# Performance work log

Hardware: AMD Instinct MI355X
Metric: run time of the kernel (lower is better)

Reference implementation:

```python
import jax, jax.numpy as jnp
import numpy as np

B, L, F, H, K = 2048, 256, 64, 32, 2  # batch, seq len, features, g_hidden, LocalHilDim

def _dense_init(key, fan_in, fan_out):
    return (jax.random.normal(key, (fan_in, fan_out), jnp.float32) / np.sqrt(fan_in).astype(np.float32))

def setup_inputs() -> dict:
    key = jax.random.key(0)
    ks = jax.random.split(key, 12)
    s = jax.random.randint(ks[0], (B, L), 0, K)
    g = jax.random.normal(ks[1], (B,), jnp.float32)
    return dict(
        s=s, g=g,
        W_emb=_dense_init(ks[2], K, F), b_emb=jnp.zeros((F,), jnp.float32),
        W_g1=_dense_init(ks[3], 1, H), b_g1=jnp.zeros((H,), jnp.float32),
        W_g2=_dense_init(ks[4], H, F), b_g2=jnp.zeros((F,), jnp.float32),
        W_gh=_dense_init(ks[5], 1, F), b_gh=jnp.zeros((F,), jnp.float32),
        W_gc=_dense_init(ks[6], 1, F), b_gc=jnp.zeros((F,), jnp.float32),
        Wi=_dense_init(ks[7], F, 4 * F),  # fused input->gates (flax LSTMCell ii/if/ig/io, no bias)
        Wh=_dense_init(ks[8], F, 4 * F),  # fused hidden->gates (hi/hf/hg/ho)
        b_lstm=jnp.zeros((4 * F,), jnp.float32),  # fused gate biases
        W_amp=_dense_init(ks[9], F, K), b_amp=jnp.zeros((K,), jnp.float32),
    )

def reference(s, g, W_emb, b_emb, W_g1, b_g1, W_g2, b_g2, W_gh, b_gh, W_gc, b_gc, Wi, Wh, b_lstm, W_amp, b_amp):
    logProbFactor = 1.0
    g_in = g[:, None]                                            # [B,1]
    g_vec = jnp.tanh(g_in @ W_g1 + b_g1) @ W_g2 + b_g2          # g_mlp -> [B,F]
    h0 = g_in @ W_gh + b_gh                                      # init_carry h [B,F]
    c0 = g_in @ W_gc + b_gc                                      # init_carry c [B,F]
    s_pad = jnp.pad(s, ((0, 0), (1, 0)))                         # [B,L+1], leading 0 token
    seqy = jax.nn.one_hot(s_pad, K, dtype=jnp.float32)           # [B,L+1,K]
    emb = seqy @ W_emb + b_emb + g_vec[:, None, :]               # [B,L+1,F]
    # precompute input-side gate projections once: [B,L+1,4F]
    x_proj = emb @ Wi + b_lstm

    def step(carry, xt):                                         # xt: [B,4F]
        h, c = carry
        z = xt + h @ Wh
        zi, zf, zg, zo = jnp.split(z, 4, axis=-1)
        c = jax.nn.sigmoid(zf) * c + jax.nn.sigmoid(zi) * jnp.tanh(zg)
        h = jax.nn.sigmoid(zo) * jnp.tanh(c)
        return (h, c), h

    _, ys = jax.lax.scan(step, (h0, c0), jnp.swapaxes(x_proj, 0, 1))  # ys: [L+1,B,F]
    y = jnp.swapaxes(ys, 0, 1)                                   # [B,L+1,F]
    logits = y[:, :-1, :] @ W_amp + b_amp                        # [B,L,K]
    logp = jax.nn.log_softmax(logits) * logProbFactor
    token_logp = jnp.take_along_axis(logp, s[..., None], axis=-1)[..., 0]  # [B,L]
    return token_logp.sum(axis=-1)                               # [B]
```

## Files before the change

kernel.cpp:

```cpp
#include <hip/hip_runtime.h>


typedef __attribute__((ext_vector_type(8))) short bf16x8;
typedef __attribute__((ext_vector_type(4))) float f32x4;

#define L2E 1.44269504088896340736f
#define LN2 0.69314718055994530942f

__device__ __forceinline__ short f2bf(float x) {
    unsigned u = __builtin_bit_cast(unsigned, x);
    unsigned r = (u + 0x7FFFu + ((u >> 16) & 1u)) >> 16;
    return (short)r;
}

__global__ __launch_bounds__(256) void lstm_kernel(
    const int* __restrict__ s, const float* __restrict__ g,
    const float* __restrict__ W_emb, const float* __restrict__ b_emb,
    const float* __restrict__ W_g1, const float* __restrict__ b_g1,
    const float* __restrict__ W_g2, const float* __restrict__ b_g2,
    const float* __restrict__ W_gh, const float* __restrict__ b_gh,
    const float* __restrict__ W_gc, const float* __restrict__ b_gc,
    const float* __restrict__ Wi, const float* __restrict__ Wh,
    const float* __restrict__ b_lstm, const float* __restrict__ W_amp,
    const float* __restrict__ b_amp, float* __restrict__ out)
{
    __shared__ float Bx[35 * 256];
    __shared__ unsigned char sp_l[260];
    __shared__ __align__(16) short Hb[2][320];
    __shared__ float red[4][4];

    const int tid = threadIdx.x;
    const int w   = tid >> 6;
    const int l   = tid & 63;
    const int n2  = l & 15;
    const int q   = l >> 4;
    const int wgb = blockIdx.x * 4;

    {
        const int n = tid;
        const float sc = (n >= 128 && n < 192) ? (-2.0f * L2E) : (-L2E);
        float acc[35];
        #pragma unroll
        for (int i = 0; i < 35; ++i) acc[i] = 0.f;
        for (int f = 0; f < 64; ++f) {
            float wi = Wi[f * 256 + n] * sc;
            #pragma unroll
            for (int k = 0; k < 32; ++k) acc[k] += W_g2[k * 64 + f] * wi;
            acc[32] += W_emb[f] * wi;
            acc[33] += W_emb[64 + f] * wi;
            acc[34] += (b_emb[f] + b_g2[f]) * wi;
        }
        acc[34] += b_lstm[n] * sc;
        #pragma unroll
        for (int i = 0; i < 35; ++i) Bx[i * 256 + n] = acc[i];
    }
    {
        unsigned v = 0;
        #pragma unroll
        for (int b = 0; b < 4; ++b)
            v |= (unsigned)(s[(wgb + b) * 256 + tid] & 1) << b;
        sp_l[tid + 1] = (unsigned char)v;
        if (tid == 0) sp_l[0] = 0;
    }
    __syncthreads();

    bf16x8 Bf[4][2];
    float  Dsel[4];
    f32x4  C0b[4];
    {
        bf16x8 B2f[4];
        float c0add[4];
        #pragma unroll
        for (int gi = 0; gi < 4; ++gi) {
            const int n = gi * 64 + w * 16 + n2;
            const float scg = (gi == 2) ? (-2.0f * L2E) : (-L2E);
            #pragma unroll
            for (int kf = 0; kf < 2; ++kf)
                #pragma unroll
                for (int j = 0; j < 8; ++j)
                    Bf[gi][kf][j] = f2bf(Wh[(kf * 32 + q * 8 + j) * 256 + n] * scg);
            #pragma unroll
            for (int j = 0; j < 8; ++j)
                B2f[gi][j] = f2bf(Bx[(q * 8 + j) * 256 + n]);
            c0add[gi] = Bx[32 * 256 + n] + Bx[34 * 256 + n];
            Dsel[gi]  = Bx[33 * 256 + n] - Bx[32 * 256 + n];
        }
        const float g_a = g[wgb + ((l >> 2) & 3)];
        bf16x8 Atv;
        #pragma unroll
        for (int j = 0; j < 8; ++j) {
            int k = q * 8 + j;
            Atv[j] = f2bf(tanhf(g_a * W_g1[k] + b_g1[k]));
        }
        const f32x4 zero4 = {0.f, 0.f, 0.f, 0.f};
        #pragma unroll
        for (int gi = 0; gi < 4; ++gi) {
            f32x4 c = __builtin_amdgcn_mfma_f32_16x16x32_bf16(Atv, B2f[gi], zero4, 0, 0, 0);
            float cv = c[0] + c0add[gi];
            C0b[gi][0] = cv; C0b[gi][1] = cv; C0b[gi][2] = cv; C0b[gi][3] = cv;
        }
    }
    bf16x8 BLd0, BLd1;
    f32x4 CL0;
    {
        #pragma unroll
        for (int j = 0; j < 8; ++j) {
            int k = q * 8 + j;
            BLd0[j] = (n2 == 0) ? f2bf(W_amp[k * 2 + 1] - W_amp[k * 2]) : (short)0;
            BLd1[j] = (n2 == 0) ? f2bf(W_amp[(k + 32) * 2 + 1] - W_amp[(k + 32) * 2]) : (short)0;
        }
        float bd = (n2 == 0) ? (b_amp[1] - b_amp[0]) : 0.f;
        CL0[0] = bd; CL0[1] = bd; CL0[2] = bd; CL0[3] = bd;
    }

    const int fcol  = w * 16 + n2;
    const int haddr = q * 80 + fcol;
    float cs;
    {
        float gb = g[wgb + q];
        cs = (-2.0f * L2E) * (gb * W_gc[fcol] + b_gc[fcol]);
        Hb[0][haddr] = f2bf(gb * W_gh[fcol] + b_gh[fcol]);
    }
    __syncthreads();

    const int ra = ((l >> 2) & 3) * 80 + q * 8;
    float slp = 0.f;
    unsigned spt = 0;

    auto step = [&](int t, int rb, int slot, bool doGate) {
        bf16x8 a0 = *(const bf16x8*)&Hb[rb][ra];
        bf16x8 a1 = *(const bf16x8*)&Hb[rb][ra + 32];
        unsigned spt_n = sp_l[t + 1];
        const unsigned bit = (spt >> q) & 1u;
        const float f_lane = (float)bit;

        f32x4 acc[4];
        #pragma unroll
        for (int gi = 0; gi < 4; ++gi) {
            f32x4 a = __builtin_amdgcn_mfma_f32_16x16x32_bf16(a1, Bf[gi][1], C0b[gi], 0, 0, 0);
            acc[gi] = __builtin_amdgcn_mfma_f32_16x16x32_bf16(a0, Bf[gi][0], a, 0, 0, 0);
        }

        const bool rr = (w == slot) && (t >= 1);
        float dL = 0.f;
        if (rr) {
            f32x4 aL = __builtin_amdgcn_mfma_f32_16x16x32_bf16(a1, BLd1, CL0, 0, 0, 0);
            aL = __builtin_amdgcn_mfma_f32_16x16x32_bf16(a0, BLd0, aL, 0, 0, 0);
            dL = aL[0];
        }

        if (doGate) {
            float yi = __builtin_fmaf(f_lane, Dsel[0], acc[0][0]);
            float yf = __builtin_fmaf(f_lane, Dsel[1], acc[1][0]);
            float yg = __builtin_fmaf(f_lane, Dsel[2], acc[2][0]);
            float yo = __builtin_fmaf(f_lane, Dsel[3], acc[3][0]);
            float si = __builtin_amdgcn_rcpf(1.0f + __builtin_amdgcn_exp2f(yi));
            float sf = __builtin_amdgcn_rcpf(1.0f + __builtin_amdgcn_exp2f(yf));
            float rg = __builtin_amdgcn_rcpf(1.0f + __builtin_amdgcn_exp2f(yg));
            float so = __builtin_amdgcn_rcpf(1.0f + __builtin_amdgcn_exp2f(yo));
            float tgs = __builtin_fmaf(-4.0f * L2E, rg, 2.0f * L2E);
            cs = __builtin_fmaf(sf, cs, si * tgs);
            float r5 = __builtin_amdgcn_rcpf(1.0f + __builtin_amdgcn_exp2f(cs));
            float th = __builtin_fmaf(2.0f, r5, -1.0f);
            float h  = so * th;
            unsigned hv;
            asm("v_cvt_pk_bf16_f32 %0, %1, %2" : "=v"(hv) : "v"(h), "v"(h));
            Hb[1 - rb][haddr] = (short)hv;
        }
        const unsigned bitc = bit;
        spt = spt_n;
        __syncthreads();

        if (rr) {
            float x = bitc ? -dL : dL;
            float e = __builtin_amdgcn_exp2f(L2E * x);
            slp -= LN2 * __builtin_amdgcn_logf(1.0f + e);
        }
    };

    for (int t0 = 0; t0 < 256; t0 += 4) {
        step(t0 + 0, 0, 0, true);
        step(t0 + 1, 1, 1, true);
        step(t0 + 2, 0, 2, true);
        step(t0 + 3, 1, 3, true);
    }
    step(256, 0, 0, false);

    if (n2 == 0) red[w][q] = slp;
    __syncthreads();
    if (tid < 4)
        out[wgb + tid] = red[0][tid] + red[1][tid] + red[2][tid] + red[3][tid];
}

extern "C" void kernel_launch(void* const* d_in, const int* in_sizes, int n_in,
                              void* d_out, int out_size, void* d_ws, size_t ws_size,
                              hipStream_t stream) {
    (void)in_sizes; (void)n_in; (void)out_size; (void)d_ws; (void)ws_size;
    const int*   s      = (const int*)d_in[0];
    const float* g      = (const float*)d_in[1];
    const float* W_emb  = (const float*)d_in[2];
    const float* b_emb  = (const float*)d_in[3];
    const float* W_g1   = (const float*)d_in[4];
    const float* b_g1   = (const float*)d_in[5];
    const float* W_g2   = (const float*)d_in[6];
    const float* b_g2   = (const float*)d_in[7];
    const float* W_gh   = (const float*)d_in[8];
    const float* b_gh   = (const float*)d_in[9];
    const float* W_gc   = (const float*)d_in[10];
    const float* b_gc   = (const float*)d_in[11];
    const float* Wi     = (const float*)d_in[12];
    const float* Wh     = (const float*)d_in[13];
    const float* b_lstm = (const float*)d_in[14];
    const float* W_amp  = (const float*)d_in[15];
    const float* b_amp  = (const float*)d_in[16];
    float* out = (float*)d_out;

    lstm_kernel<<<512, 256, 0, stream>>>(s, g, W_emb, b_emb, W_g1, b_g1, W_g2, b_g2,
                                         W_gh, b_gh, W_gc, b_gc, Wi, Wh, b_lstm,
                                         W_amp, b_amp, out);
}
```

Measured before the change: 200.1 us.

## Process eight batch rows per workgroup using unused MFMA output rows

Each workgroup now handles 8 sequences instead of 4, filling more rows of the 16x16 MFMA (each lane now computes two batch rows, A and B, taken from accumulator elements 0 and 2). The grid is halved to 256 blocks, which on a 256-CU part gives one block per CU and removes the second wave of blocks. The cost is twice the gate arithmetic per lane on the serial recurrence path and lower occupancy per CU, with launch_bounds set to 1 block.

```diff
diff --git a/kernel.cpp b/kernel.cpp
--- a/kernel.cpp
+++ b/kernel.cpp
@@ -13,7 +13,7 @@
     return (short)r;
 }
 
-__global__ __launch_bounds__(256) void lstm_kernel(
+__global__ __launch_bounds__(256, 1) void lstm_kernel(
     const int* __restrict__ s, const float* __restrict__ g,
     const float* __restrict__ W_emb, const float* __restrict__ b_emb,
     const float* __restrict__ W_g1, const float* __restrict__ b_g1,
@@ -26,15 +26,15 @@
 {
     __shared__ float Bx[35 * 256];
     __shared__ unsigned char sp_l[260];
-    __shared__ __align__(16) short Hb[2][320];
-    __shared__ float red[4][4];
+    __shared__ __align__(16) short Hb[2][640];
+    __shared__ float red[4][8];
 
     const int tid = threadIdx.x;
     const int w   = tid >> 6;
     const int l   = tid & 63;
     const int n2  = l & 15;
     const int q   = l >> 4;
-    const int wgb = blockIdx.x * 4;
+    const int wgb = blockIdx.x * 8;
 
     {
         const int n = tid;
@@ -57,7 +57,7 @@
     {
         unsigned v = 0;
         #pragma unroll
-        for (int b = 0; b < 4; ++b)
+        for (int b = 0; b < 8; ++b)
             v |= (unsigned)(s[(wgb + b) * 256 + tid] & 1) << b;
         sp_l[tid + 1] = (unsigned char)v;
         if (tid == 0) sp_l[0] = 0;
@@ -85,7 +85,7 @@
             c0add[gi] = Bx[32 * 256 + n] + Bx[34 * 256 + n];
             Dsel[gi]  = Bx[33 * 256 + n] - Bx[32 * 256 + n];
         }
-        const float g_a = g[wgb + ((l >> 2) & 3)];
+        const float g_a = g[wgb + ((l & 15) >> 1)];
         bf16x8 Atv;
         #pragma unroll
         for (int j = 0; j < 8; ++j) {
@@ -96,8 +96,9 @@
         #pragma unroll
         for (int gi = 0; gi < 4; ++gi) {
             f32x4 c = __builtin_amdgcn_mfma_f32_16x16x32_bf16(Atv, B2f[gi], zero4, 0, 0, 0);
-            float cv = c[0] + c0add[gi];
-            C0b[gi][0] = cv; C0b[gi][1] = cv; C0b[gi][2] = cv; C0b[gi][3] = cv;
+            float cvA = c[0] + c0add[gi];
+            float cvB = c[2] + c0add[gi];
+            C0b[gi][0] = cvA; C0b[gi][1] = cvA; C0b[gi][2] = cvB; C0b[gi][3] = cvB;
         }
     }
     bf16x8 BLd0, BLd1;
@@ -113,26 +114,32 @@
         CL0[0] = bd; CL0[1] = bd; CL0[2] = bd; CL0[3] = bd;
     }
 
-    const int fcol  = w * 16 + n2;
-    const int haddr = q * 80 + fcol;
-    float cs;
-    {
-        float gb = g[wgb + q];
-        cs = (-2.0f * L2E) * (gb * W_gc[fcol] + b_gc[fcol]);
-        Hb[0][haddr] = f2bf(gb * W_gh[fcol] + b_gh[fcol]);
+    const int fcol   = w * 16 + n2;
+    const int bA     = q * 2;
+    const int bB     = bA + 1;
+    const int haddrA = bA * 80 + fcol;
+    const int haddrB = haddrA + 80;
+    float csA, csB;
+    {
+        float gA = g[wgb + bA], gB = g[wgb + bB];
+        csA = (-2.0f * L2E) * (gA * W_gc[fcol] + b_gc[fcol]);
+        csB = (-2.0f * L2E) * (gB * W_gc[fcol] + b_gc[fcol]);
+        Hb[0][haddrA] = f2bf(gA * W_gh[fcol] + b_gh[fcol]);
+        Hb[0][haddrB] = f2bf(gB * W_gh[fcol] + b_gh[fcol]);
     }
     __syncthreads();
 
-    const int ra = ((l >> 2) & 3) * 80 + q * 8;
-    float slp = 0.f;
+    const int ra = ((l & 15) >> 1) * 80 + q * 8;
+    float slpA = 0.f, slpB = 0.f;
     unsigned spt = 0;
 
     auto step = [&](int t, int rb, int slot, bool doGate) {
         bf16x8 a0 = *(const bf16x8*)&Hb[rb][ra];
         bf16x8 a1 = *(const bf16x8*)&Hb[rb][ra + 32];
         unsigned spt_n = sp_l[t + 1];
-        const unsigned bit = (spt >> q) & 1u;
-        const float f_lane = (float)bit;
+        const unsigned bitA = (spt >> bA) & 1u;
+        const unsigned bitB = (spt >> bB) & 1u;
+        const float fA = (float)bitA, fB = (float)bitB;
 
         f32x4 acc[4];
         #pragma unroll
@@ -142,39 +149,56 @@
         }
 
         const bool rr = (w == slot) && (t >= 1);
-        float dL = 0.f;
+        float dLA = 0.f, dLB = 0.f;
         if (rr) {
             f32x4 aL = __builtin_amdgcn_mfma_f32_16x16x32_bf16(a1, BLd1, CL0, 0, 0, 0);
             aL = __builtin_amdgcn_mfma_f32_16x16x32_bf16(a0, BLd0, aL, 0, 0, 0);
-            dL = aL[0];
+            dLA = aL[0]; dLB = aL[2];
         }
 
         if (doGate) {
-            float yi = __builtin_fmaf(f_lane, Dsel[0], acc[0][0]);
-            float yf = __builtin_fmaf(f_lane, Dsel[1], acc[1][0]);
-            float yg = __builtin_fmaf(f_lane, Dsel[2], acc[2][0]);
-            float yo = __builtin_fmaf(f_lane, Dsel[3], acc[3][0]);
-            float si = __builtin_amdgcn_rcpf(1.0f + __builtin_amdgcn_exp2f(yi));
-            float sf = __builtin_amdgcn_rcpf(1.0f + __builtin_amdgcn_exp2f(yf));
-            float rg = __builtin_amdgcn_rcpf(1.0f + __builtin_amdgcn_exp2f(yg));
-            float so = __builtin_amdgcn_rcpf(1.0f + __builtin_amdgcn_exp2f(yo));
-            float tgs = __builtin_fmaf(-4.0f * L2E, rg, 2.0f * L2E);
-            cs = __builtin_fmaf(sf, cs, si * tgs);
-            float r5 = __builtin_amdgcn_rcpf(1.0f + __builtin_amdgcn_exp2f(cs));
-            float th = __builtin_fmaf(2.0f, r5, -1.0f);
-            float h  = so * th;
+            float yiA = __builtin_fmaf(fA, Dsel[0], acc[0][0]);
+            float yiB = __builtin_fmaf(fB, Dsel[0], acc[0][2]);
+            float yfA = __builtin_fmaf(fA, Dsel[1], acc[1][0]);
+            float yfB = __builtin_fmaf(fB, Dsel[1], acc[1][2]);
+            float ygA = __builtin_fmaf(fA, Dsel[2], acc[2][0]);
+            float ygB = __builtin_fmaf(fB, Dsel[2], acc[2][2]);
+            float yoA = __builtin_fmaf(fA, Dsel[3], acc[3][0]);
+            float yoB = __builtin_fmaf(fB, Dsel[3], acc[3][2]);
+            float siA = __builtin_amdgcn_rcpf(1.0f + __builtin_amdgcn_exp2f(yiA));
+            float siB = __builtin_amdgcn_rcpf(1.0f + __builtin_amdgcn_exp2f(yiB));
+            float sfA = __builtin_amdgcn_rcpf(1.0f + __builtin_amdgcn_exp2f(yfA));
+            float sfB = __builtin_amdgcn_rcpf(1.0f + __builtin_amdgcn_exp2f(yfB));
+            float rgA = __builtin_amdgcn_rcpf(1.0f + __builtin_amdgcn_exp2f(ygA));
+            float rgB = __builtin_amdgcn_rcpf(1.0f + __builtin_amdgcn_exp2f(ygB));
+            float soA = __builtin_amdgcn_rcpf(1.0f + __builtin_amdgcn_exp2f(yoA));
+            float soB = __builtin_amdgcn_rcpf(1.0f + __builtin_amdgcn_exp2f(yoB));
+            float tgsA = __builtin_fmaf(-4.0f * L2E, rgA, 2.0f * L2E);
+            float tgsB = __builtin_fmaf(-4.0f * L2E, rgB, 2.0f * L2E);
+            csA = __builtin_fmaf(sfA, csA, siA * tgsA);
+            csB = __builtin_fmaf(sfB, csB, siB * tgsB);
+            float r5A = __builtin_amdgcn_rcpf(1.0f + __builtin_amdgcn_exp2f(csA));
+            float r5B = __builtin_amdgcn_rcpf(1.0f + __builtin_amdgcn_exp2f(csB));
+            float thA = __builtin_fmaf(2.0f, r5A, -1.0f);
+            float thB = __builtin_fmaf(2.0f, r5B, -1.0f);
+            float hA  = soA * thA;
+            float hB  = soB * thB;
             unsigned hv;
-            asm("v_cvt_pk_bf16_f32 %0, %1, %2" : "=v"(hv) : "v"(h), "v"(h));
-            Hb[1 - rb][haddr] = (short)hv;
-        }
-        const unsigned bitc = bit;
+            asm("v_cvt_pk_bf16_f32 %0, %1, %2" : "=v"(hv) : "v"(hA), "v"(hB));
+            Hb[1 - rb][haddrA] = (short)hv;
+            Hb[1 - rb][haddrB] = (short)(hv >> 16);
+        }
+        const unsigned bAc = bitA, bBc = bitB;
         spt = spt_n;
         __syncthreads();
 
         if (rr) {
-            float x = bitc ? -dL : dL;
-            float e = __builtin_amdgcn_exp2f(L2E * x);
-            slp -= LN2 * __builtin_amdgcn_logf(1.0f + e);
+            float xA = bAc ? -dLA : dLA;
+            float xB = bBc ? -dLB : dLB;
+            float eA = __builtin_amdgcn_exp2f(L2E * xA);
+            float eB = __builtin_amdgcn_exp2f(L2E * xB);
+            slpA -= LN2 * __builtin_amdgcn_logf(1.0f + eA);
+            slpB -= LN2 * __builtin_amdgcn_logf(1.0f + eB);
         }
     };
 
@@ -186,9 +210,9 @@
     }
     step(256, 0, 0, false);
 
-    if (n2 == 0) red[w][q] = slp;
+    if (n2 == 0) { red[w][bA] = slpA; red[w][bB] = slpB; }
     __syncthreads();
-    if (tid < 4)
+    if (tid < 8)
         out[wgb + tid] = red[0][tid] + red[1][tid] + red[2][tid] + red[3][tid];
 }
 
@@ -215,7 +239,7 @@
     const float* b_amp  = (const float*)d_in[16];
     float* out = (float*)d_out;
 
-    lstm_kernel<<<512, 256, 0, stream>>>(s, g, W_emb, b_emb, W_g1, b_g1, W_g2, b_g2,
+    lstm_kernel<<<256, 256, 0, stream>>>(s, g, W_emb, b_emb, W_g1, b_g1, W_g2, b_g2,
                                          W_gh, b_gh, W_gc, b_gc, Wi, Wh, b_lstm,
                                          W_amp, b_amp, out);
 }
```

Result: faster. 195.5 us (-2.3%).
